# Kernel optimization log

Hardware: AMD Instinct MI355X
Metric: run time of the kernel (lower is better)

Reference implementation:

```python
import jax, jax.numpy as jnp
import numpy as np

B = 8192       # batch
HID = 1024     # hidden_dim
HEADS = 8      # head_count
OBS, ACT, N_AGENTS = 128, 32, 4
ENC_IN = N_AGENTS * OBS + ACT   # 544
DEC_IN = (N_AGENTS - 1) * ACT   # 96


def _linear(key, fan_in, fan_out):
    k1, k2 = jax.random.split(key)
    lim = 1.0 / np.sqrt(fan_in)
    W = jax.random.uniform(k1, (fan_in, fan_out), minval=-lim, maxval=lim, dtype=jnp.float32)
    b = jax.random.uniform(k2, (fan_out,), minval=-lim, maxval=lim, dtype=jnp.float32)
    return W, b


def setup_inputs() -> dict:
    key = jax.random.key(0)
    ks = jax.random.split(key, 10)
    s = jax.random.normal(ks[0], (B, N_AGENTS * OBS), dtype=jnp.float32)
    a = jax.random.normal(ks[1], (B, N_AGENTS * ACT), dtype=jnp.float32)
    W_enc_in, b_enc_in = _linear(ks[2], ENC_IN, HID)   # encoder_input_fc
    W_dec_in, b_dec_in = _linear(ks[3], DEC_IN, HID)   # decoder_input_fc
    W_eh, b_eh = _linear(ks[4], HID, HID)              # fc_encoder_input
    head_ks = jax.random.split(ks[5], HEADS)
    Wb = [_linear(k, HID, HID) for k in head_ks]       # fc_encoder_heads
    W_heads = jnp.stack([w for w, _ in Wb], axis=0)    # [H, HID, HID]
    b_heads = jnp.stack([b for _, b in Wb], axis=0)    # [H, HID]
    W_dh, b_dh = _linear(ks[6], HID, HID)              # fc_decoder_input
    W1, b1 = _linear(ks[7], HID, HID)                  # fc1
    W2, b2 = _linear(ks[8], HID, 1)                    # fc2
    return {"s": s, "a": a,
            "W_enc_in": W_enc_in, "b_enc_in": b_enc_in,
            "W_dec_in": W_dec_in, "b_dec_in": b_dec_in,
            "W_eh": W_eh, "b_eh": b_eh,
            "W_heads": W_heads, "b_heads": b_heads,
            "W_dh": W_dh, "b_dh": b_dh,
            "W1": W1, "b1": b1, "W2": W2, "b2": b2}


def reference(s, a, W_enc_in, b_enc_in, W_dec_in, b_dec_in, W_eh, b_eh,
              W_heads, b_heads, W_dh, b_dh, W1, b1, W2, b2):
    relu = jax.nn.relu
    # agent id = 0: own action is a[:, :ACT], others' actions are a[:, ACT:]
    enc_input = jnp.concatenate([s, a[:, :ACT]], axis=1) @ W_enc_in + b_enc_in   # [B, HID]
    dec_input = a[:, ACT:] @ W_dec_in + b_dec_in                                 # [B, HID]
    # Attention_ATT_2
    encoder_h = relu(enc_input @ W_eh + b_eh)                                    # [B, HID]
    encoder_heads = relu(jnp.einsum('bd,hde->hbe', encoder_h, W_heads)
                         + b_heads[:, None, :])                                  # [H, B, HID]
    decoder_H = relu(dec_input @ W_dh + b_dh)                                    # [B, HID]
    scores = jnp.einsum('hbd,bd->bh', encoder_heads, decoder_H)                  # [B, H]
    attn = jax.nn.softmax(scores, axis=1)                                        # [B, H]
    context = jnp.einsum('hbd,bh->bd', encoder_heads, attn)                      # [B, HID]
    x = relu(context @ W1 + b1)
    q = x @ W2 + b2                                                              # [B, 1]
    return q
```

## Files before the change

### kernel.cpp

```cpp
#include <hip/hip_runtime.h>
#include <hip/hip_bf16.h>
#include <hip/hip_fp16.h>

#define BATCH   8192
#define HID     1024
#define HEADS   8
#define BC      2048

typedef unsigned int  u32;
typedef unsigned short u16;
typedef __attribute__((ext_vector_type(8))) short bf16x8;
typedef __attribute__((ext_vector_type(4))) float f32x4;

__device__ __forceinline__ u32 pack_hi2(u32 u0, u32 u1) {
    return (u0 >> 16) | (u1 & 0xFFFF0000u);
}
__device__ __forceinline__ void split1(float x, u16& h, u16& l) {
    const u32 u = __float_as_uint(x);
    h = (u16)(u >> 16);
    const float r = x - __uint_as_float(u & 0xFFFF0000u);
    l = (u16)(__float_as_uint(r) >> 16);
}
__device__ __forceinline__ void splitA4(float4 v, uint2& hi, uint2& lo) {
    u32 u0 = __float_as_uint(v.x), u1 = __float_as_uint(v.y),
        u2 = __float_as_uint(v.z), u3 = __float_as_uint(v.w);
    float r0 = v.x - __uint_as_float(u0 & 0xFFFF0000u);
    float r1 = v.y - __uint_as_float(u1 & 0xFFFF0000u);
    float r2 = v.z - __uint_as_float(u2 & 0xFFFF0000u);
    float r3 = v.w - __uint_as_float(u3 & 0xFFFF0000u);
    hi.x = pack_hi2(u0, u1);
    hi.y = pack_hi2(u2, u3);
    lo.x = pack_hi2(__float_as_uint(r0), __float_as_uint(r1));
    lo.y = pack_hi2(__float_as_uint(r2), __float_as_uint(r3));
}

__device__ __forceinline__ void gld16(const u16* g, u16* l) {
    __builtin_amdgcn_global_load_lds(
        (const __attribute__((address_space(1))) u32*)g,
        (__attribute__((address_space(3))) u32*)l, 16, 0, 0);
}

#define SCHED0 __builtin_amdgcn_sched_barrier(0)

struct WSplitArgs {
    const float* src[6];
    u16* hi[6];
    u16* lo[6];
};

__global__ __launch_bounds__(256) void split_weight_all(WSplitArgs args)
{
    const int z = blockIdx.z;
    int which, zz = 0;
    if (z < 3)       { which = z; }
    else if (z < 11) { which = 3; zz = z - 3; }
    else             { which = z - 7; }
    const int KT = (which == 4) ? 17 : (which == 5 ? 3 : 32);
    const int kt = blockIdx.x;
    if (kt >= KT) return;
    const int K = KT * 32;
    const long long zoff = (long long)zz * K * 1024;
    const float* W  = args.src[which] + zoff;
    u16* hi = args.hi[which] + zoff;
    u16* lo = args.lo[which] + zoff;

    const int n0  = blockIdx.y * 128;
    const int tid = threadIdx.x;
    const int k   = tid >> 3;
    const int ng  = (tid & 7) * 16;
    const float* src = W + (long long)(kt * 32 + k) * 1024 + n0 + ng;
    u16* dh = hi + ((long long)kt * 1024 + n0) * 32 + k;
    u16* dl = lo + ((long long)kt * 1024 + n0) * 32 + k;
#pragma unroll
    for (int t = 0; t < 4; t++) {
        const float4 v = *(const float4*)(src + t * 4);
        u16 h0, l0, h1, l1, h2, l2, h3, l3;
        split1(v.x, h0, l0); split1(v.y, h1, l1);
        split1(v.z, h2, l2); split1(v.w, h3, l3);
        const int nb = (ng + t * 4) * 32;
        dh[nb]      = h0; dl[nb]      = l0;
        dh[nb + 32] = h1; dl[nb + 32] = l1;
        dh[nb + 64] = h2; dl[nb + 64] = l2;
        dh[nb + 96] = h3; dl[nb + 96] = l3;
    }
}

#define MFMA_Q24(AH_, AL_, IB, JB) \
    __builtin_amdgcn_s_setprio(1); \
    _Pragma("unroll") \
    for (int i_ = 0; i_ < 4; i_++) \
        _Pragma("unroll") \
        for (int j_ = 0; j_ < 2; j_++) \
            acc[(IB) + i_][(JB) + j_] = __builtin_amdgcn_mfma_f32_16x16x32_bf16(AH_[i_], bh[(JB) + j_], acc[(IB) + i_][(JB) + j_], 0, 0, 0); \
    _Pragma("unroll") \
    for (int i_ = 0; i_ < 4; i_++) \
        _Pragma("unroll") \
        for (int j_ = 0; j_ < 2; j_++) \
            acc[(IB) + i_][(JB) + j_] = __builtin_amdgcn_mfma_f32_16x16x32_bf16(AH_[i_], bl[(JB) + j_], acc[(IB) + i_][(JB) + j_], 0, 0, 0); \
    _Pragma("unroll") \
    for (int i_ = 0; i_ < 4; i_++) \
        _Pragma("unroll") \
        for (int j_ = 0; j_ < 2; j_++) \
            acc[(IB) + i_][(JB) + j_] = __builtin_amdgcn_mfma_f32_16x16x32_bf16(AL_[i_], bh[(JB) + j_], acc[(IB) + i_][(JB) + j_], 0, 0, 0); \
    __builtin_amdgcn_s_setprio(0);

#define G_GEOM \
    const int tid  = threadIdx.x; \
    const int lane = tid & 63; \
    const int wv   = tid >> 6; \
    const int wm   = wv >> 1, wn = wv & 1; \
    const int m0   = blockIdx.y * 256; \
    const int n0   = blockIdx.x * 128; \
    const int fr   = lane & 15; \
    const int fq   = lane >> 4; \
    const int lro2 = (lane >> 2) * 32 + (((lane & 3) ^ ((lane >> 3) & 3)) * 8); \
    const int fqx2 = (fq ^ ((fr >> 1) & 3)) * 8; \
    const int wrA  = wv * 32; \
    const int wrB  = wv * 16;

#define G_STAGE_A(buf_, t_) { \
    u16* d_ = (buf_); \
    const long long ao_ = abase + (long long)(t_) * astep; \
    gld16(Ahp + ao_ + (long long)wrA * 32 + lro2, d_ + wrA * 32); \
    gld16(Ahp + ao_ + (long long)(wrA + 16) * 32 + lro2, d_ + (wrA + 16) * 32); \
    gld16(Alp + ao_ + (long long)wrA * 32 + lro2, d_ + 8192 + wrA * 32); \
    gld16(Alp + ao_ + (long long)(wrA + 16) * 32 + lro2, d_ + 8192 + (wrA + 16) * 32); }

#define G_STAGE_B(buf_, t_) { \
    u16* d_ = (buf_); \
    const long long bo_ = bbase + (long long)(t_) * 32768; \
    gld16(Bhp + bo_ + (long long)wrB * 32 + lro2, d_ + 16384 + wrB * 32); \
    gld16(Blp + bo_ + (long long)wrB * 32 + lro2, d_ + 20480 + wrB * 32); }

#define G_RD_A(AH_, AL_, bp_) \
    _Pragma("unroll") \
    for (int i_ = 0; i_ < 4; i_++) { \
        const int off_ = (wm * 64 + i_ * 16 + fr) * 32 + fqx2; \
        AH_[i_] = *(const bf16x8*)((bp_) + off_); \
        AL_[i_] = *(const bf16x8*)((bp_) + 8192 + off_); }

#define G_RD_B(bp_, JB) \
    _Pragma("unroll") \
    for (int j_ = 0; j_ < 2; j_++) { \
        const int off_ = (wn * 64 + ((JB) + j_) * 16 + fr) * 32 + fqx2; \
        bh[(JB) + j_] = *(const bf16x8*)((bp_) + 16384 + off_); \
        bl[(JB) + j_] = *(const bf16x8*)((bp_) + 20480 + off_); }

#define G_TILE(t_, AH_, AL_, NAH_, NAL_) { \
    const u16* bp = smem + ((t_) % 3) * 24576; \
    u16* nb2 = smem + (((t_) + 2) % 3) * 24576; \
    const u16* np = smem + (((t_) + 1) % 3) * 24576; \
    const bool s_ = (t_) + 2 < KT; \
    const bool p_ = (t_) + 1 < KT; \
    G_RD_B(bp, 2) \
    if (s_) { G_STAGE_A(nb2, (t_) + 2); G_STAGE_B(nb2, (t_) + 2); } \
    SCHED0; \
    MFMA_Q24(AH_, AL_, 0, 0) \
    asm volatile("s_waitcnt lgkmcnt(0)" ::: "memory"); \
    if (s_) { asm volatile("s_waitcnt vmcnt(6)" ::: "memory"); } \
    else    { asm volatile("s_waitcnt vmcnt(0)" ::: "memory"); } \
    __builtin_amdgcn_s_barrier(); \
    SCHED0; \
    if (p_) { G_RD_A(NAH_, NAL_, np) G_RD_B(np, 0) } \
    SCHED0; \
    MFMA_Q24(AH_, AL_, 0, 2) \
    SCHED0; \
}

template <int RELU, int OUTP>
__global__ __launch_bounds__(512, 2) void gemm_fast(
    const u16* __restrict__ Ahp, const u16* __restrict__ Alp, int MA, int moff,
    const u16* __restrict__ Bhp, const u16* __restrict__ Blp,
    const float* __restrict__ bias,
    float* __restrict__ Cf,
    u16* __restrict__ Chp, u16* __restrict__ Clp, int MC,
    int K)
{
    __shared__ alignas(16) u16 smem[3 * 24576];
    G_GEOM

    f32x4 acc[4][4];
#pragma unroll
    for (int i = 0; i < 4; i++)
#pragma unroll
        for (int j = 0; j < 4; j++) acc[i][j] = 0;

    const int KT = K >> 5;
    const long long astep = (long long)MA * 32;
    const long long abase = ((long long)moff + m0) * 32;
    const long long bbase = (long long)n0 * 32;

    bf16x8 ahA[4], alA[4], ahB[4], alB[4], bh[4], bl[4];

    G_STAGE_A(smem, 0); G_STAGE_B(smem, 0);
    G_STAGE_A(smem + 24576, 1); G_STAGE_B(smem + 24576, 1);
    asm volatile("s_waitcnt vmcnt(6)" ::: "memory");
    __builtin_amdgcn_s_barrier();
    SCHED0;
    G_RD_A(ahA, alA, smem)
    G_RD_B(smem, 0)

    for (int t = 0; t < KT; t += 2) {
        G_TILE(t,     ahA, alA, ahB, alB)
        G_TILE(t + 1, ahB, alB, ahA, alA)
    }

#pragma unroll
    for (int j = 0; j < 4; j++) {
        const int n = n0 + wn * 64 + j * 16 + fr;
        const float bb = bias[n];
#pragma unroll
        for (int i = 0; i < 4; i++) {
#pragma unroll
            for (int r = 0; r < 4; r++) {
                const int m = m0 + wm * 64 + i * 16 + fq * 4 + r;
                float v = acc[i][j][r] + bb;
                if (RELU) v = fmaxf(v, 0.0f);
                if (OUTP) {
                    u16 h, l;
                    split1(v, h, l);
                    const long long d = ((long long)(n >> 5) * MC + moff + m) * 32 + (n & 31);
                    Chp[d] = h;
                    Clp[d] = l;
                } else {
                    Cf[(long long)m * 1024 + n] = v;
                }
            }
        }
    }
}

#define H_STAGE_A(buf_, t_) { \
    u16* d_ = (buf_); \
    const long long ao_ = abase + (long long)(t_) * astep; \
    gld16(Ahp + ao_ + (long long)wrA * 32 + lro2, d_ + wrA * 32); \
    gld16(Ahp + ao_ + (long long)(wrA + 16) * 32 + lro2, d_ + (wrA + 16) * 32); \
    gld16(Alp + ao_ + (long long)wrA * 32 + lro2, d_ + 8192 + wrA * 32); \
    gld16(Alp + ao_ + (long long)(wrA + 16) * 32 + lro2, d_ + 8192 + (wrA + 16) * 32); }

#define H_STAGE_B(buf_, t_) { \
    u16* d_ = (buf_); \
    const long long bo_ = bbase + (long long)(t_) * 32768; \
    gld16(Bhp + bo_ + (long long)wrA * 32 + lro2, d_ + 16384 + wrA * 32); \
    gld16(Bhp + bo_ + (long long)(wrA + 16) * 32 + lro2, d_ + 16384 + (wrA + 16) * 32); \
    gld16(Blp + bo_ + (long long)wrA * 32 + lro2, d_ + 24576 + wrA * 32); \
    gld16(Blp + bo_ + (long long)(wrA + 16) * 32 + lro2, d_ + 24576 + (wrA + 16) * 32); }

#define H_RD_A0(bp_) \
    _Pragma("unroll") \
    for (int i_ = 0; i_ < 4; i_++) { \
        const int off_ = (wm * 128 + i_ * 16 + fr) * 32 + fqx2; \
        ah0[i_] = *(const bf16x8*)((bp_) + off_); \
        al0[i_] = *(const bf16x8*)((bp_) + 8192 + off_); }

#define H_RD_A1(bp_) \
    _Pragma("unroll") \
    for (int i_ = 0; i_ < 4; i_++) { \
        const int off_ = (wm * 128 + 64 + i_ * 16 + fr) * 32 + fqx2; \
        ah1[i_] = *(const bf16x8*)((bp_) + off_); \
        al1[i_] = *(const bf16x8*)((bp_) + 8192 + off_); }

#define H_RD_B01(bp_) \
    _Pragma("unroll") \
    for (int j_ = 0; j_ < 2; j_++) { \
        const int off_ = (wn * 64 + j_ * 16 + fr) * 32 + fqx2; \
        bh[j_] = *(const bf16x8*)((bp_) + 16384 + off_); \
        bl[j_] = *(const bf16x8*)((bp_) + 24576 + off_); }

#define H_RD_B23(bp_) \
    _Pragma("unroll") \
    for (int j_ = 0; j_ < 2; j_++) { \
        const int off_ = (wn * 64 + (2 + j_) * 16 + fr) * 32 + fqx2; \
        bh[2 + j_] = *(const bf16x8*)((bp_) + 16384 + off_); \
        bl[2 + j_] = *(const bf16x8*)((bp_) + 24576 + off_); }

__global__ __launch_bounds__(512, 2) void heads_kernel(
    const u16* __restrict__ Ahp, const u16* __restrict__ Alp, int MA, int moff,
    const u16* __restrict__ Whp, const u16* __restrict__ Wlp,
    const float* __restrict__ b_heads,
    const float* __restrict__ decH,
    __half* __restrict__ headsb,
    float* __restrict__ scoresp)
{
    __shared__ alignas(16) u16 smem[2 * 32768];
    __shared__ float scred[4][256];
    const int tid  = threadIdx.x;
    const int lane = tid & 63;
    const int wv   = tid >> 6;
    const int wm   = wv >> 2;
    const int wn   = wv & 3;
    const int fr   = lane & 15;
    const int fq   = lane >> 4;
    const int m0   = blockIdx.y * 256;
    const int n0   = blockIdx.x * 256;
    const int lro2 = (lane >> 2) * 32 + (((lane & 3) ^ ((lane >> 3) & 3)) * 8);
    const int fqx2 = (fq ^ ((fr >> 1) & 3)) * 8;
    const int wrA  = wv * 32;
    const int h = blockIdx.z;
    const u16* Bhp = Whp + (long long)h * 1048576;
    const u16* Blp = Wlp + (long long)h * 1048576;
    const float* bias = b_heads + h * 1024;

    f32x4 acc[8][4];
#pragma unroll
    for (int i = 0; i < 8; i++)
#pragma unroll
        for (int j = 0; j < 4; j++) acc[i][j] = 0;

    const long long astep = (long long)MA * 32;
    const long long abase = ((long long)moff + m0) * 32;
    const long long bbase = (long long)n0 * 32;

    bf16x8 ah0[4], al0[4], ah1[4], al1[4], bh[4], bl[4];

    H_STAGE_A(smem, 0);
    H_STAGE_B(smem, 0);
    asm volatile("s_waitcnt vmcnt(0)" ::: "memory");
    __builtin_amdgcn_s_barrier();
    SCHED0;
    H_RD_A0(smem)
    H_RD_B01(smem)

    for (int t = 0; t < 32; t++) {
        const u16* bp = smem + (t & 1) * 32768;
        u16* nb = smem + ((t + 1) & 1) * 32768;
        const bool more = t < 31;
        H_RD_B23(bp)
        if (more) H_STAGE_A(nb, t + 1);
        SCHED0;
        MFMA_Q24(ah0, al0, 0, 0)
        SCHED0;
        H_RD_A1(bp)
        if (more) H_STAGE_B(nb, t + 1);
        SCHED0;
        MFMA_Q24(ah0, al0, 0, 2)
        SCHED0;
        MFMA_Q24(ah1, al1, 4, 0)
        asm volatile("s_waitcnt lgkmcnt(0)" ::: "memory");
        asm volatile("s_waitcnt vmcnt(0)" ::: "memory");
        __builtin_amdgcn_s_barrier();
        SCHED0;
        if (more) { H_RD_A0(nb) H_RD_B01(nb) }
        SCHED0;
        MFMA_Q24(ah1, al1, 4, 2)
        SCHED0;
    }

    float part[8][4];
#pragma unroll
    for (int i = 0; i < 8; i++)
#pragma unroll
        for (int r = 0; r < 4; r++) part[i][r] = 0.0f;

#pragma unroll
    for (int j = 0; j < 4; j++) {
        const int n = n0 + wn * 64 + j * 16 + fr;
        const float bb = bias[n];
#pragma unroll
        for (int i = 0; i < 8; i++) {
#pragma unroll
            for (int r = 0; r < 4; r++) {
                const int b_loc = m0 + wm * 128 + i * 16 + fq * 4 + r;
                const float v = fmaxf(acc[i][j][r] + bb, 0.0f);
                part[i][r] = fmaf(v, decH[(long long)b_loc * 1024 + n], part[i][r]);
            }
        }
    }

#pragma unroll
    for (int pss = 0; pss < 2; pss++) {
        __syncthreads();
        if (wm == pss) {
#pragma unroll
            for (int j = 0; j < 4; j++) {
                const int n = n0 + wn * 64 + j * 16 + fr;
                const float bb = bias[n];
#pragma unroll
                for (int i = 0; i < 8; i++) {
#pragma unroll
                    for (int r = 0; r < 4; r++) {
                        const float v = fmaxf(acc[i][j][r] + bb, 0.0f);
                        smem[(i * 16 + fq * 4 + r) * 260 + wn * 64 + j * 16 + fr] =
                            __half_as_ushort(__float2half(v));
                    }
                }
            }
        }
        __syncthreads();
#pragma unroll
        for (int it = 0; it < 16; it++) {
            const int row = it * 8 + wv;
            const uint2 d = *(const uint2*)(smem + row * 260 + lane * 4);
            __half* hb = headsb + ((long long)(m0 + pss * 128 + row) * HEADS + h) * 1024
                       + n0 + lane * 4;
            *(uint2*)hb = d;
        }
    }

#pragma unroll
    for (int off = 1; off < 16; off <<= 1)
#pragma unroll
        for (int i = 0; i < 8; i++)
#pragma unroll
            for (int r = 0; r < 4; r++)
                part[i][r] += __shfl_xor(part[i][r], off, 64);

    if (fr == 0) {
#pragma unroll
        for (int i = 0; i < 8; i++)
#pragma unroll
            for (int r = 0; r < 4; r++)
                scred[wn][wm * 128 + i * 16 + fq * 4 + r] = part[i][r];
    }
    __syncthreads();
    if (tid < 256) {
        const float sv = scred[0][tid] + scred[1][tid] + scred[2][tid] + scred[3][tid];
        scoresp[(long long)(h * 4 + blockIdx.x) * BC + m0 + tid] = sv;
    }
}

template <int RELU>
__global__ __launch_bounds__(256) void gemm_cvt(
    const float* __restrict__ src1, int lda1, int kofs1,
    const float* __restrict__ src2, int lda2, int ksplit,
    const u16* __restrict__ Bhp, const u16* __restrict__ Blp,
    const float* __restrict__ bias,
    u16* __restrict__ Chp, u16* __restrict__ Clp, int MC,
    int K)
{
    __shared__ alignas(16) u16 Ah[4096], Al[4096], Bh[4096], Bl[4096];
    const int tid  = threadIdx.x;
    const int lane = tid & 63;
    const int wv   = tid >> 6;
    const int wm   = wv >> 1, wn = wv & 1;
    const int fr   = lane & 15;
    const int fq   = lane >> 4;
    const int m0   = blockIdx.y * 128;
    const int n0   = blockIdx.x * 128;
    const int fqx  = (fq ^ (fr & 3)) * 8;
    const int lro  = (lane >> 2) * 32 + (((lane & 3) ^ ((lane >> 2) & 3)) * 8);
    const int br0  = wv * 16;
    const int br1  = 64 + wv * 16;
    const int ar   = tid >> 3;
    const int akq  = tid & 7;
    const int awoff = (((akq >> 1) ^ (ar & 3)) * 8) + (akq & 1) * 4;

    f32x4 acc[4][4];
#pragma unroll
    for (int i = 0; i < 4; i++)
#pragma unroll
        for (int j = 0; j < 4; j++) acc[i][j] = 0;

    const int KT = K >> 5;
    for (int kt = 0; kt < KT; kt++) {
        const int k0 = kt * 32;
        const float* srcp; int ldk, kc;
        if (k0 < ksplit) { srcp = src1; ldk = lda1; kc = k0 + kofs1; }
        else             { srcp = src2; ldk = lda2; kc = k0 - ksplit; }

        const u16* Bg  = Bhp + ((long long)kt * 1024 + n0) * 32;
        const u16* Bg2 = Blp + ((long long)kt * 1024 + n0) * 32;
        gld16(Bg  + br0 * 32 + lro, &Bh[br0 * 32]);
        gld16(Bg  + br1 * 32 + lro, &Bh[br1 * 32]);
        gld16(Bg2 + br0 * 32 + lro, &Bl[br0 * 32]);
        gld16(Bg2 + br1 * 32 + lro, &Bl[br1 * 32]);

#pragma unroll
        for (int it = 0; it < 4; it++) {
            const int row = ar + it * 32;
            const float4 v = *(const float4*)(srcp + (long long)(m0 + row) * ldk + kc + akq * 4);
            uint2 hi, lo;
            splitA4(v, hi, lo);
            *(uint2*)&Ah[row * 32 + awoff] = hi;
            *(uint2*)&Al[row * 32 + awoff] = lo;
        }
        __syncthreads();

        bf16x8 ah[4], al[4], bh[4], bl[4];
#pragma unroll
        for (int i = 0; i < 4; i++) {
            const int off = (wm * 64 + i * 16 + fr) * 32 + fqx;
            ah[i] = *(const bf16x8*)&Ah[off];
            al[i] = *(const bf16x8*)&Al[off];
        }
#pragma unroll
        for (int j = 0; j < 4; j++) {
            const int off = (wn * 64 + j * 16 + fr) * 32 + fqx;
            bh[j] = *(const bf16x8*)&Bh[off];
            bl[j] = *(const bf16x8*)&Bl[off];
        }
#pragma unroll
        for (int i = 0; i < 4; i++)
#pragma unroll
            for (int j = 0; j < 4; j++) {
                acc[i][j] = __builtin_amdgcn_mfma_f32_16x16x32_bf16(ah[i], bh[j], acc[i][j], 0, 0, 0);
                acc[i][j] = __builtin_amdgcn_mfma_f32_16x16x32_bf16(ah[i], bl[j], acc[i][j], 0, 0, 0);
                acc[i][j] = __builtin_amdgcn_mfma_f32_16x16x32_bf16(al[i], bh[j], acc[i][j], 0, 0, 0);
            }
        __syncthreads();
    }

#pragma unroll
    for (int j = 0; j < 4; j++) {
        const int n = n0 + wn * 64 + j * 16 + fr;
        const float bb = bias[n];
#pragma unroll
        for (int i = 0; i < 4; i++) {
#pragma unroll
            for (int r = 0; r < 4; r++) {
                const int m = m0 + wm * 64 + i * 16 + fq * 4 + r;
                float v = acc[i][j][r] + bb;
                if (RELU) v = fmaxf(v, 0.0f);
                u16 h, l;
                split1(v, h, l);
                const long long d = ((long long)(n >> 5) * MC + m) * 32 + (n & 31);
                Chp[d] = h;
                Clp[d] = l;
            }
        }
    }
}

__global__ __launch_bounds__(256) void context_kernel(
    const __half* __restrict__ headsb, const float* __restrict__ scoresp,
    u16* __restrict__ ctx_hi, u16* __restrict__ ctx_lo, int MC, int row0)
{
    __shared__ float sc_s[32];
    __shared__ float attn_s[HEADS];
    const int b = blockIdx.x;
    const int tid = threadIdx.x;
    if (tid < 32) sc_s[tid] = scoresp[(long long)tid * BC + b];
    __syncthreads();
    if (tid == 0) {
        float sc[HEADS];
#pragma unroll
        for (int h = 0; h < HEADS; h++) {
            float s = 0.0f;
#pragma unroll
            for (int nt = 0; nt < 4; nt++) s += sc_s[h * 4 + nt];
            sc[h] = s;
        }
        float mx = sc[0];
#pragma unroll
        for (int h = 1; h < HEADS; h++) mx = fmaxf(mx, sc[h]);
        float e[HEADS], sum = 0.0f;
#pragma unroll
        for (int h = 0; h < HEADS; h++) { e[h] = __expf(sc[h] - mx); sum += e[h]; }
        const float inv = 1.0f / sum;
#pragma unroll
        for (int h = 0; h < HEADS; h++) attn_s[h] = e[h] * inv;
    }
    __syncthreads();

    const int d = tid * 4;
    float w[HEADS];
#pragma unroll
    for (int h = 0; h < HEADS; h++) w[h] = attn_s[h];
    float4 acc = make_float4(0.f, 0.f, 0.f, 0.f);
#pragma unroll
    for (int h = 0; h < HEADS; h++) {
        const __half2* hp = (const __half2*)(headsb + ((long long)b * HEADS + h) * 1024 + d);
        const float2 f0 = __half22float2(hp[0]);
        const float2 f1 = __half22float2(hp[1]);
        acc.x = fmaf(w[h], f0.x, acc.x);
        acc.y = fmaf(w[h], f0.y, acc.y);
        acc.z = fmaf(w[h], f1.x, acc.z);
        acc.w = fmaf(w[h], f1.y, acc.w);
    }
    uint2 hi, lo;
    splitA4(acc, hi, lo);
    const long long off = ((long long)(d >> 5) * MC + row0 + b) * 32 + (d & 31);
    *(uint2*)(ctx_hi + off) = hi;
    *(uint2*)(ctx_lo + off) = lo;
}

__global__ __launch_bounds__(256) void fc2_kernel(
    const float* __restrict__ x, const float* __restrict__ W2,
    const float* __restrict__ b2, float* __restrict__ q)
{
    const int b   = blockIdx.x;
    const int tid = threadIdx.x;
    __shared__ float red[4];

    const float4 xv = *(const float4*)(x + (long long)b * 1024 + tid * 4);
    const float4 wv = *(const float4*)(W2 + tid * 4);
    float p = xv.x * wv.x + xv.y * wv.y + xv.z * wv.z + xv.w * wv.w;
#pragma unroll
    for (int off = 32; off > 0; off >>= 1) p += __shfl_down(p, off, 64);
    if ((tid & 63) == 0) red[tid >> 6] = p;
    __syncthreads();
    if (tid == 0) q[b] = red[0] + red[1] + red[2] + red[3] + b2[0];
}

extern "C" void kernel_launch(void* const* d_in, const int* in_sizes, int n_in,
                              void* d_out, int out_size, void* d_ws, size_t ws_size,
                              hipStream_t stream)
{
    const float* s        = (const float*)d_in[0];
    const float* a        = (const float*)d_in[1];
    const float* W_enc_in = (const float*)d_in[2];
    const float* b_enc_in = (const float*)d_in[3];
    const float* W_dec_in = (const float*)d_in[4];
    const float* b_dec_in = (const float*)d_in[5];
    const float* W_eh     = (const float*)d_in[6];
    const float* b_eh     = (const float*)d_in[7];
    const float* W_heads  = (const float*)d_in[8];
    const float* b_heads  = (const float*)d_in[9];
    const float* W_dh     = (const float*)d_in[10];
    const float* b_dh     = (const float*)d_in[11];
    const float* W1       = (const float*)d_in[12];
    const float* b1       = (const float*)d_in[13];
    const float* W2       = (const float*)d_in[14];
    const float* b2       = (const float*)d_in[15];
    float* q_out = (float*)d_out;

    u16* P = (u16*)d_ws;
    u16* enc_hi = P; P += 557056;
    u16* enc_lo = P; P += 557056;
    u16* dec_hi = P; P += 98304;
    u16* dec_lo = P; P += 98304;
    u16* eh_hi  = P; P += 1048576;
    u16* eh_lo  = P; P += 1048576;
    u16* dh_hi  = P; P += 1048576;
    u16* dh_lo  = P; P += 1048576;
    u16* w1_hi  = P; P += 1048576;
    u16* w1_lo  = P; P += 1048576;
    u16* wh_hi  = P; P += 8388608;
    u16* wh_lo  = P; P += 8388608;
    char* act = (char*)P;

    const dim3 blk(256);
    const dim3 blk512(512);

    WSplitArgs wa;
    wa.src[0] = W_eh;    wa.hi[0] = eh_hi;  wa.lo[0] = eh_lo;
    wa.src[1] = W_dh;    wa.hi[1] = dh_hi;  wa.lo[1] = dh_lo;
    wa.src[2] = W1;      wa.hi[2] = w1_hi;  wa.lo[2] = w1_lo;
    wa.src[3] = W_heads; wa.hi[3] = wh_hi;  wa.lo[3] = wh_lo;
    wa.src[4] = W_enc_in; wa.hi[4] = enc_hi; wa.lo[4] = enc_lo;
    wa.src[5] = W_dec_in; wa.hi[5] = dec_hi; wa.lo[5] = dec_lo;
    split_weight_all<<<dim3(32, 8, 13), blk, 0, stream>>>(wa);

    const bool high = (ws_size >= 150011904ULL);

    if (high) {
        u16*    bufA_hi = (u16*)act;
        u16*    bufA_lo = bufA_hi + 8388608;
        __half* headsb  = (__half*)act;
        u16*    encH_hi = (u16*)(act + 33554432);
        u16*    encH_lo = encH_hi + 8388608;
        float*  decH    = (float*)(act + 2LL * 33554432);
        float*  scoresp = (float*)(act + 3LL * 33554432);

        const dim3 ggc(8, 64, 1);
        const dim3 ggf(8, 32, 1);
        gemm_cvt<0><<<ggc, blk, 0, stream>>>(s, 512, 0, a, 128, 512,
            enc_hi, enc_lo, b_enc_in, bufA_hi, bufA_lo, 8192, 544);
        gemm_fast<1, 1><<<ggf, blk512, 0, stream>>>(bufA_hi, bufA_lo, 8192, 0,
            eh_hi, eh_lo, b_eh, nullptr, encH_hi, encH_lo, 8192, 1024);
        gemm_cvt<0><<<ggc, blk, 0, stream>>>(a, 128, 32, a, 128, 1 << 28,
            dec_hi, dec_lo, b_dec_in, bufA_hi, bufA_lo, 8192, 96);
        gemm_fast<1, 0><<<ggf, blk512, 0, stream>>>(bufA_hi, bufA_lo, 8192, 0,
            dh_hi, dh_lo, b_dh, decH, nullptr, nullptr, 0, 1024);

        for (int c = 0; c < BATCH / BC; c++) {
            heads_kernel<<<dim3(4, BC / 256, 8), blk512, 0, stream>>>(
                encH_hi, encH_lo, 8192, c * BC, wh_hi, wh_lo, b_heads,
                decH + (long long)c * BC * 1024, headsb, scoresp);
            context_kernel<<<dim3(BC), blk, 0, stream>>>(
                headsb, scoresp, encH_hi, encH_lo, 8192, c * BC);
        }
        gemm_fast<1, 0><<<ggf, blk512, 0, stream>>>(encH_hi, encH_lo, 8192, 0,
            w1_hi, w1_lo, b1, decH, nullptr, nullptr, 0, 1024);
        fc2_kernel<<<dim3(BATCH), blk, 0, stream>>>(decH, W2, b2, q_out);
    } else {
        __half* headsb  = (__half*)act;
        u16*    bufA_hi = (u16*)act;
        u16*    bufA_lo = bufA_hi + 2097152;
        u16*    encH_hi = (u16*)(act + 33554432);
        u16*    encH_lo = encH_hi + 2097152;
        float*  decH    = (float*)(act + 33554432 + 8388608);
        float*  scoresp = (float*)(act + 33554432 + 2LL * 8388608);

        const dim3 ggc(8, BC / 128, 1);
        const dim3 ggf(8, BC / 256, 1);
        for (int c = 0; c < BATCH / BC; c++) {
            const float* sC = s + (long long)c * BC * 512;
            const float* aC = a + (long long)c * BC * 128;
            gemm_cvt<0><<<ggc, blk, 0, stream>>>(sC, 512, 0, aC, 128, 512,
                enc_hi, enc_lo, b_enc_in, bufA_hi, bufA_lo, BC, 544);
            gemm_fast<1, 1><<<ggf, blk512, 0, stream>>>(bufA_hi, bufA_lo, BC, 0,
                eh_hi, eh_lo, b_eh, nullptr, encH_hi, encH_lo, BC, 1024);
            gemm_cvt<0><<<ggc, blk, 0, stream>>>(aC, 128, 32, aC, 128, 1 << 28,
                dec_hi, dec_lo, b_dec_in, bufA_hi, bufA_lo, BC, 96);
            gemm_fast<1, 0><<<ggf, blk512, 0, stream>>>(bufA_hi, bufA_lo, BC, 0,
                dh_hi, dh_lo, b_dh, decH, nullptr, nullptr, 0, 1024);
            heads_kernel<<<dim3(4, BC / 256, 8), blk512, 0, stream>>>(
                encH_hi, encH_lo, BC, 0, wh_hi, wh_lo, b_heads,
                decH, headsb, scoresp);
            context_kernel<<<dim3(BC), blk, 0, stream>>>(
                headsb, scoresp, encH_hi, encH_lo, BC, 0);
            gemm_fast<1, 0><<<ggf, blk512, 0, stream>>>(encH_hi, encH_lo, BC, 0,
                w1_hi, w1_lo, b1, decH, nullptr, nullptr, 0, 1024);
            fc2_kernel<<<dim3(BC), blk, 0, stream>>>(decH, W2, b2, q_out + (long long)c * BC);
        }
    }
}
```

Baseline: 696.9 us.

## Fuse fc2 dot-product into fc1 GEMM epilogue with atomic reduction

The fc1 GEMM epilogue now applies bias and ReLU and multiplies by W2 directly. Each block reduces its partial dot products across lanes with shuffles and atomically adds them into q, which is zeroed by a memset up front. This removes the fc1 activation write, the fc2 read and one kernel launch. Separately, the heads kernel issues its B-tile stage loads alongside the A-tile loads earlier in the loop. The atomics make the summation order nondeterministic.

```diff
diff --git a/kernel.cpp b/kernel.cpp
--- a/kernel.cpp
+++ b/kernel.cpp
@@ -174,7 +174,9 @@
     const float* __restrict__ bias,
     float* __restrict__ Cf,
     u16* __restrict__ Chp, u16* __restrict__ Clp, int MC,
-    int K)
+    int K,
+    const float* __restrict__ W2v, const float* __restrict__ b2v,
+    float* __restrict__ qout)
 {
     __shared__ alignas(16) u16 smem[3 * 24576];
     G_GEOM
@@ -205,6 +207,47 @@
         G_TILE(t + 1, ahB, alB, ahA, alA)
     }
 
+    if (OUTP == 2) {
+        float part[4][4];
+#pragma unroll
+        for (int i = 0; i < 4; i++)
+#pragma unroll
+            for (int r = 0; r < 4; r++) part[i][r] = 0.0f;
+#pragma unroll
+        for (int j = 0; j < 4; j++) {
+            const int n = n0 + wn * 64 + j * 16 + fr;
+            const float bb = bias[n];
+            const float w2 = W2v[n];
+#pragma unroll
+            for (int i = 0; i < 4; i++) {
+#pragma unroll
+                for (int r = 0; r < 4; r++) {
+                    const float v = fmaxf(acc[i][j][r] + bb, 0.0f);
+                    part[i][r] = fmaf(v, w2, part[i][r]);
+                }
+            }
+        }
+#pragma unroll
+        for (int off = 1; off < 16; off <<= 1)
+#pragma unroll
+            for (int i = 0; i < 4; i++)
+#pragma unroll
+                for (int r = 0; r < 4; r++)
+                    part[i][r] += __shfl_xor(part[i][r], off, 64);
+        if (fr == 0) {
+            const float extra = (blockIdx.x == 0 && wn == 0) ? b2v[0] : 0.0f;
+#pragma unroll
+            for (int i = 0; i < 4; i++) {
+#pragma unroll
+                for (int r = 0; r < 4; r++) {
+                    const int m = m0 + wm * 64 + i * 16 + fq * 4 + r;
+                    atomicAdd(&qout[m], part[i][r] + extra);
+                }
+            }
+        }
+        return;
+    }
+
 #pragma unroll
     for (int j = 0; j < 4; j++) {
         const int n = n0 + wn * 64 + j * 16 + fr;
@@ -216,7 +259,7 @@
                 const int m = m0 + wm * 64 + i * 16 + fq * 4 + r;
                 float v = acc[i][j][r] + bb;
                 if (RELU) v = fmaxf(v, 0.0f);
-                if (OUTP) {
+                if (OUTP == 1) {
                     u16 h, l;
                     split1(v, h, l);
                     const long long d = ((long long)(n >> 5) * MC + moff + m) * 32 + (n & 31);
@@ -326,12 +369,11 @@
         u16* nb = smem + ((t + 1) & 1) * 32768;
         const bool more = t < 31;
         H_RD_B23(bp)
-        if (more) H_STAGE_A(nb, t + 1);
+        if (more) { H_STAGE_A(nb, t + 1); H_STAGE_B(nb, t + 1); }
         SCHED0;
         MFMA_Q24(ah0, al0, 0, 0)
         SCHED0;
         H_RD_A1(bp)
-        if (more) H_STAGE_B(nb, t + 1);
         SCHED0;
         MFMA_Q24(ah0, al0, 0, 2)
         SCHED0;
@@ -574,24 +616,6 @@
     *(uint2*)(ctx_lo + off) = lo;
 }
 
-__global__ __launch_bounds__(256) void fc2_kernel(
-    const float* __restrict__ x, const float* __restrict__ W2,
-    const float* __restrict__ b2, float* __restrict__ q)
-{
-    const int b   = blockIdx.x;
-    const int tid = threadIdx.x;
-    __shared__ float red[4];
-
-    const float4 xv = *(const float4*)(x + (long long)b * 1024 + tid * 4);
-    const float4 wv = *(const float4*)(W2 + tid * 4);
-    float p = xv.x * wv.x + xv.y * wv.y + xv.z * wv.z + xv.w * wv.w;
-#pragma unroll
-    for (int off = 32; off > 0; off >>= 1) p += __shfl_down(p, off, 64);
-    if ((tid & 63) == 0) red[tid >> 6] = p;
-    __syncthreads();
-    if (tid == 0) q[b] = red[0] + red[1] + red[2] + red[3] + b2[0];
-}
-
 extern "C" void kernel_launch(void* const* d_in, const int* in_sizes, int n_in,
                               void* d_out, int out_size, void* d_ws, size_t ws_size,
                               hipStream_t stream)
@@ -632,6 +656,8 @@
     const dim3 blk(256);
     const dim3 blk512(512);
 
+    hipMemsetAsync(q_out, 0, BATCH * sizeof(float), stream);
+
     WSplitArgs wa;
     wa.src[0] = W_eh;    wa.hi[0] = eh_hi;  wa.lo[0] = eh_lo;
     wa.src[1] = W_dh;    wa.hi[1] = dh_hi;  wa.lo[1] = dh_lo;
@@ -657,11 +683,13 @@
         gemm_cvt<0><<<ggc, blk, 0, stream>>>(s, 512, 0, a, 128, 512,
             enc_hi, enc_lo, b_enc_in, bufA_hi, bufA_lo, 8192, 544);
         gemm_fast<1, 1><<<ggf, blk512, 0, stream>>>(bufA_hi, bufA_lo, 8192, 0,
-            eh_hi, eh_lo, b_eh, nullptr, encH_hi, encH_lo, 8192, 1024);
+            eh_hi, eh_lo, b_eh, nullptr, encH_hi, encH_lo, 8192, 1024,
+            nullptr, nullptr, nullptr);
         gemm_cvt<0><<<ggc, blk, 0, stream>>>(a, 128, 32, a, 128, 1 << 28,
             dec_hi, dec_lo, b_dec_in, bufA_hi, bufA_lo, 8192, 96);
         gemm_fast<1, 0><<<ggf, blk512, 0, stream>>>(bufA_hi, bufA_lo, 8192, 0,
-            dh_hi, dh_lo, b_dh, decH, nullptr, nullptr, 0, 1024);
+            dh_hi, dh_lo, b_dh, decH, nullptr, nullptr, 0, 1024,
+            nullptr, nullptr, nullptr);
 
         for (int c = 0; c < BATCH / BC; c++) {
             heads_kernel<<<dim3(4, BC / 256, 8), blk512, 0, stream>>>(
@@ -670,9 +698,9 @@
             context_kernel<<<dim3(BC), blk, 0, stream>>>(
                 headsb, scoresp, encH_hi, encH_lo, 8192, c * BC);
         }
-        gemm_fast<1, 0><<<ggf, blk512, 0, stream>>>(encH_hi, encH_lo, 8192, 0,
-            w1_hi, w1_lo, b1, decH, nullptr, nullptr, 0, 1024);
-        fc2_kernel<<<dim3(BATCH), blk, 0, stream>>>(decH, W2, b2, q_out);
+        gemm_fast<1, 2><<<ggf, blk512, 0, stream>>>(encH_hi, encH_lo, 8192, 0,
+            w1_hi, w1_lo, b1, nullptr, nullptr, nullptr, 0, 1024,
+            W2, b2, q_out);
     } else {
         __half* headsb  = (__half*)act;
         u16*    bufA_hi = (u16*)act;
@@ -690,19 +718,21 @@
             gemm_cvt<0><<<ggc, blk, 0, stream>>>(sC, 512, 0, aC, 128, 512,
                 enc_hi, enc_lo, b_enc_in, bufA_hi, bufA_lo, BC, 544);
             gemm_fast<1, 1><<<ggf, blk512, 0, stream>>>(bufA_hi, bufA_lo, BC, 0,
-                eh_hi, eh_lo, b_eh, nullptr, encH_hi, encH_lo, BC, 1024);
+                eh_hi, eh_lo, b_eh, nullptr, encH_hi, encH_lo, BC, 1024,
+                nullptr, nullptr, nullptr);
             gemm_cvt<0><<<ggc, blk, 0, stream>>>(aC, 128, 32, aC, 128, 1 << 28,
                 dec_hi, dec_lo, b_dec_in, bufA_hi, bufA_lo, BC, 96);
             gemm_fast<1, 0><<<ggf, blk512, 0, stream>>>(bufA_hi, bufA_lo, BC, 0,
-                dh_hi, dh_lo, b_dh, decH, nullptr, nullptr, 0, 1024);
+                dh_hi, dh_lo, b_dh, decH, nullptr, nullptr, 0, 1024,
+                nullptr, nullptr, nullptr);
             heads_kernel<<<dim3(4, BC / 256, 8), blk512, 0, stream>>>(
                 encH_hi, encH_lo, BC, 0, wh_hi, wh_lo, b_heads,
                 decH, headsb, scoresp);
             context_kernel<<<dim3(BC), blk, 0, stream>>>(
                 headsb, scoresp, encH_hi, encH_lo, BC, 0);
-            gemm_fast<1, 0><<<ggf, blk512, 0, stream>>>(encH_hi, encH_lo, BC, 0,
-                w1_hi, w1_lo, b1, decH, nullptr, nullptr, 0, 1024);
-            fc2_kernel<<<dim3(BC), blk, 0, stream>>>(decH, W2, b2, q_out + (long long)c * BC);
-        }
-    }
-}
+            gemm_fast<1, 2><<<ggf, blk512, 0, stream>>>(encH_hi, encH_lo, BC, 0,
+                w1_hi, w1_lo, b1, nullptr, nullptr, nullptr, 0, 1024,
+                W2, b2, q_out + (long long)c * BC);
+        }
+    }
+}
```

After: 674.1 us, median of 2. -3.3%, faster.
